# Kernel tuning notes

Measured on AMD Instinct MI355X. Metric: run time of the kernel, lower is better.

The kernel has to match this reference:

```python
import jax, jax.numpy as jnp
import numpy as np

B, D, K, NDIM = 4, 81, 2048, 4  # batch, feature dim, n mixture components, box coord dims


def setup_inputs() -> dict:
    key = jax.random.key(0)
    k1, k2, k3, k4 = jax.random.split(key, 4)
    x = jax.random.normal(k1, (B, D, K), dtype=jnp.float32)
    # mixture weights, positive and normalized over components
    pi = jax.nn.softmax(jax.random.normal(k2, (B, 1, K), dtype=jnp.float32), axis=2)
    # component means in [0,1] (normalized box coords)
    mu = jax.random.uniform(k3, (B, NDIM, K), dtype=jnp.float32)
    # positive scales
    sig = jax.random.uniform(k4, (B, NDIM, K), dtype=jnp.float32) * 0.1 + 0.01
    return {"x": x, "pi": pi, "mu": mu, "sig": sig}


def _cauchy_pdf(mu, sig, points):
    # mu, sig: (B, 1, NDIM, K); points: (B, P, NDIM, 1)
    d = points - mu
    return sig / (jnp.pi * (d * d + sig * sig))


def reference(x, pi, mu, sig):
    # points = mu.transpose(1,2): evaluate the mixture at each component mean
    points = jnp.transpose(mu, (0, 2, 1))            # (B, K, NDIM)
    comp = _cauchy_pdf(mu[:, None, :, :], sig[:, None, :, :],
                       points[:, :, :, None])        # (B, K, NDIM, K)
    comp = jnp.prod(comp, axis=2)                    # independent dims -> (B, K, K)
    lh = pi * comp                                   # pi (B,1,K) broadcasts over points
    coef = lh / jnp.sum(lh, axis=2, keepdims=True)   # normalize over components
    coef = jax.lax.stop_gradient(coef)               # coef_detach=True
    y = jnp.einsum('bdk,bkm->bdm', x, coef)          # torch.bmm(x, coef)
    return y
```

## Files before the change

### kernel.cpp

```cpp
#include <hip/hip_runtime.h>


typedef float v4f __attribute__((ext_vector_type(4)));
typedef float f32x4 __attribute__((ext_vector_type(4)));
typedef short bf16x8 __attribute__((ext_vector_type(8)));

namespace {
constexpr int BB = 4;
constexpr int DD = 81;
constexpr int KK = 2048;
constexpr int MROWS = 96;
constexpr float INV_PI4 = 1.0f / 97.40909103400243f;

constexpr size_t OFF_XBF = 0;
constexpr size_t OFF_RSP = (size_t)BB * MROWS * KK * 2;
}

__device__ __forceinline__ unsigned short f2bf(float f) {
    union { float f; unsigned int u; } v; v.f = f;
    unsigned int u = v.u;
    unsigned int r = (u + 0x7FFFu + ((u >> 16) & 1u)) >> 16;
    return (unsigned short)r;
}

__global__ __launch_bounds__(256, 4) void rowsum_kernel(const float* __restrict__ pi_,
                                                        const float* __restrict__ mu,
                                                        const float* __restrict__ sig,
                                                        float* __restrict__ rowsumPart) {
    __shared__ v4f   mush[256];
    __shared__ v4f   s2sh[256];
    __shared__ float csh[256];
    __shared__ float red[4][64];

    int blk = blockIdx.x;
    int b   = blk >> 8;
    int pc  = (blk & 255) >> 3;
    int ms  = blk & 7;
    int p0  = pc * 64;
    int m0  = ms * 256;
    int t   = threadIdx.x;
    int lane = t & 63, w = t >> 6;

    const float* mub = mu  + (size_t)b * 4 * KK;
    const float* sgb = sig + (size_t)b * 4 * KK;
    const float* pib = pi_ + (size_t)b * KK;

    {
        int m = m0 + t;
        v4f mm = {mub[m], mub[KK + m], mub[2 * KK + m], mub[3 * KK + m]};
        v4f sg = {sgb[m], sgb[KK + m], sgb[2 * KK + m], sgb[3 * KK + m]};
        mush[t] = mm;
        s2sh[t] = sg * sg;
        csh[t]  = pib[m] * ((sg.x * sg.y) * (sg.z * sg.w)) * INV_PI4;
    }
    int p = p0 + lane;
    v4f mp = {mub[p], mub[KK + p], mub[2 * KK + p], mub[3 * KK + p]};
    __syncthreads();

    float sum = 0.f;
#pragma unroll 8
    for (int i = 0; i < 64; ++i) {
        int mi = w * 64 + i;
        v4f d = mp - mush[mi];
        v4f q = d * d + s2sh[mi];
        float den = (q.x * q.y) * (q.z * q.w);
        sum += csh[mi] * __builtin_amdgcn_rcpf(den);
    }

    red[w][lane] = sum;
    __syncthreads();
    if (t < 64)
        rowsumPart[((size_t)(b * 8 + ms)) * KK + p0 + t] =
            red[0][t] + red[1][t] + red[2][t] + red[3][t];
}

__global__ __launch_bounds__(256) void xbf_kernel(const float* __restrict__ x,
                                                  const float* __restrict__ rowsumPart,
                                                  unsigned short* __restrict__ xbf) {
    int d = blockIdx.x;
    int b = blockIdx.y;
    int t = threadIdx.x;
    unsigned short* orow = xbf + ((size_t)(b * MROWS + d)) * KK;
    const float* xrow = x + ((size_t)(b * DD + d)) * KK;
    const float* rsp  = rowsumPart + (size_t)b * 8 * KK;
#pragma unroll
    for (int j = 0; j < 8; ++j) {
        int p = j * 256 + t;
        float rs = 0.f;
#pragma unroll
        for (int s = 0; s < 8; ++s) rs += rsp[(size_t)s * KK + p];
        float v = 0.f;
        if (d < DD) v = xrow[p] * __builtin_amdgcn_rcpf(rs);
        orow[p] = f2bf(v);
    }
}

__global__ __launch_bounds__(512, 2) void gemm_kernel(const float* __restrict__ pi_,
                                                      const float* __restrict__ mu,
                                                      const float* __restrict__ sig,
                                                      const unsigned short* __restrict__ xbf,
                                                      float* __restrict__ out) {
    __shared__ __align__(16) char smem2[49152];
    v4f* mus = (v4f*)smem2;
    f32x4 (*red)[6][64] = (f32x4 (*)[6][64])smem2;

    int t = threadIdx.x;
    int w = t >> 6, lane = t & 63;
    int r = lane & 15, q = lane >> 4;
    int b  = blockIdx.y;
    int m0 = blockIdx.x * 16;

    const float* mub = mu  + (size_t)b * 4 * KK;
    const float* sgb = sig + (size_t)b * 4 * KK;

    for (int i = t; i < KK; i += 512)
        mus[i] = (v4f){mub[i], mub[KK + i], mub[2 * KK + i], mub[3 * KK + i]};

    int m = m0 + r;
    v4f mm = {mub[m], mub[KK + m], mub[2 * KK + m], mub[3 * KK + m]};
    v4f sg = {sgb[m], sgb[KK + m], sgb[2 * KK + m], sgb[3 * KK + m]};
    v4f s2 = sg * sg;
    float cm = pi_[(size_t)b * KK + m] * ((sg.x * sg.y) * (sg.z * sg.w)) * INV_PI4;

    const unsigned short* Abase = xbf + ((size_t)(b * MROWS + r)) * KK;

    f32x4 acc[6];
#pragma unroll
    for (int i = 0; i < 6; ++i) acc[i] = (f32x4)0.f;

    __syncthreads();

    int pw = w * 256;

    bf16x8 Af[6];
#pragma unroll
    for (int Mt = 0; Mt < 6; ++Mt)
        Af[Mt] = *(const bf16x8*)(Abase + (size_t)Mt * 16 * KK + pw + q * 8);

#pragma unroll
    for (int ks = 0; ks < 8; ++ks) {
        int pb = pw + ks * 32 + q * 8;

        bf16x8 Afn[6];
        if (ks < 7) {
            int pbn = pb + 32;
#pragma unroll
            for (int Mt = 0; Mt < 6; ++Mt)
                Afn[Mt] = *(const bf16x8*)(Abase + (size_t)Mt * 16 * KK + pbn);
        }

        bf16x8 Bf;
#pragma unroll
        for (int j = 0; j < 8; ++j) {
            v4f mp = mus[pb + j];
            v4f dd = mp - mm;
            v4f qq = dd * dd + s2;
            float den = (qq.x * qq.y) * (qq.z * qq.w);
            float lh = cm * __builtin_amdgcn_rcpf(den);
            Bf[j] = (short)f2bf(lh);
        }

#pragma unroll
        for (int Mt = 0; Mt < 6; ++Mt)
            acc[Mt] = __builtin_amdgcn_mfma_f32_16x16x32_bf16(Af[Mt], Bf, acc[Mt], 0, 0, 0);

        if (ks < 7) {
#pragma unroll
            for (int Mt = 0; Mt < 6; ++Mt)
                Af[Mt] = Afn[Mt];
        }
    }

    __syncthreads();
#pragma unroll
    for (int Mt = 0; Mt < 6; ++Mt)
        red[w][Mt][lane] = acc[Mt];
    __syncthreads();

    int col = t & 15;
    int dr  = t >> 4;
#pragma unroll
    for (int k = 0; k < 3; ++k) {
        int d = dr + 32 * k;
        if (d < DD) {
            int Mt  = d >> 4;
            int row = d & 15;
            int l   = (row >> 2) * 16 + col;
            int j   = row & 3;
            float s = 0.f;
#pragma unroll
            for (int ww = 0; ww < 8; ++ww) s += red[ww][Mt][l][j];
            out[((size_t)(b * DD + d)) * KK + m0 + col] = s;
        }
    }
}

extern "C" void kernel_launch(void* const* d_in, const int* in_sizes, int n_in,
                              void* d_out, int out_size, void* d_ws, size_t ws_size,
                              hipStream_t stream) {
    const float* x   = (const float*)d_in[0];
    const float* pi_ = (const float*)d_in[1];
    const float* mu  = (const float*)d_in[2];
    const float* sig = (const float*)d_in[3];
    float* out = (float*)d_out;

    unsigned short* xbf = (unsigned short*)((char*)d_ws + OFF_XBF);
    float* rowsumPart   = (float*)((char*)d_ws + OFF_RSP);

    rowsum_kernel<<<1024, 256, 0, stream>>>(pi_, mu, sig, rowsumPart);
    dim3 xg(MROWS, BB);
    xbf_kernel<<<xg, 256, 0, stream>>>(x, rowsumPart, xbf);
    dim3 gg(KK / 16, BB);
    gemm_kernel<<<gg, 512, 0, stream>>>(pi_, mu, sig, xbf, out);
}
```

Baseline: 100.9 us.

## Fuse rowsum and x-normalization into one prep kernel per 16-point tile

Replaces the separate rowsum kernel (partial sums written to workspace) and the xbf scaling kernel with a single prep kernel. Each block owns 16 points, loops over all 2048 components in chunks staged through shared memory, reduces the row sum in shared memory, then scales and converts the matching x columns to bf16. This drops one launch and the partial-sum round trip through global memory. In exchange each block reloads all mu/sig/pi, and the x reads and bf16 writes become strided per 16-column tile, which coalesces less well.

```diff
diff --git a/kernel.cpp b/kernel.cpp
--- a/kernel.cpp
+++ b/kernel.cpp
@@ -13,7 +13,6 @@
 constexpr float INV_PI4 = 1.0f / 97.40909103400243f;
 
 constexpr size_t OFF_XBF = 0;
-constexpr size_t OFF_RSP = (size_t)BB * MROWS * KK * 2;
 }
 
 __device__ __forceinline__ unsigned short f2bf(float f) {
@@ -23,75 +22,72 @@
     return (unsigned short)r;
 }
 
-__global__ __launch_bounds__(256, 4) void rowsum_kernel(const float* __restrict__ pi_,
-                                                        const float* __restrict__ mu,
-                                                        const float* __restrict__ sig,
-                                                        float* __restrict__ rowsumPart) {
+__global__ __launch_bounds__(256) void prep_kernel(const float* __restrict__ x,
+                                                   const float* __restrict__ pi_,
+                                                   const float* __restrict__ mu,
+                                                   const float* __restrict__ sig,
+                                                   unsigned short* __restrict__ xbf) {
     __shared__ v4f   mush[256];
     __shared__ v4f   s2sh[256];
     __shared__ float csh[256];
-    __shared__ float red[4][64];
-
-    int blk = blockIdx.x;
-    int b   = blk >> 8;
-    int pc  = (blk & 255) >> 3;
-    int ms  = blk & 7;
-    int p0  = pc * 64;
-    int m0  = ms * 256;
-    int t   = threadIdx.x;
-    int lane = t & 63, w = t >> 6;
+    __shared__ float sums[16][17];
+    __shared__ float invr[16];
+
+    int b  = blockIdx.y;
+    int p0 = blockIdx.x * 16;
+    int t  = threadIdx.x;
+    int pl = t & 15;
+    int mg = t >> 4;
 
     const float* mub = mu  + (size_t)b * 4 * KK;
     const float* sgb = sig + (size_t)b * 4 * KK;
     const float* pib = pi_ + (size_t)b * KK;
 
-    {
-        int m = m0 + t;
-        v4f mm = {mub[m], mub[KK + m], mub[2 * KK + m], mub[3 * KK + m]};
-        v4f sg = {sgb[m], sgb[KK + m], sgb[2 * KK + m], sgb[3 * KK + m]};
-        mush[t] = mm;
-        s2sh[t] = sg * sg;
-        csh[t]  = pib[m] * ((sg.x * sg.y) * (sg.z * sg.w)) * INV_PI4;
-    }
-    int p = p0 + lane;
+    int p = p0 + pl;
     v4f mp = {mub[p], mub[KK + p], mub[2 * KK + p], mub[3 * KK + p]};
-    __syncthreads();
 
     float sum = 0.f;
-#pragma unroll 8
-    for (int i = 0; i < 64; ++i) {
-        int mi = w * 64 + i;
-        v4f d = mp - mush[mi];
-        v4f q = d * d + s2sh[mi];
-        float den = (q.x * q.y) * (q.z * q.w);
-        sum += csh[mi] * __builtin_amdgcn_rcpf(den);
-    }
-
-    red[w][lane] = sum;
-    __syncthreads();
-    if (t < 64)
-        rowsumPart[((size_t)(b * 8 + ms)) * KK + p0 + t] =
-            red[0][t] + red[1][t] + red[2][t] + red[3][t];
-}
-
-__global__ __launch_bounds__(256) void xbf_kernel(const float* __restrict__ x,
-                                                  const float* __restrict__ rowsumPart,
-                                                  unsigned short* __restrict__ xbf) {
-    int d = blockIdx.x;
-    int b = blockIdx.y;
-    int t = threadIdx.x;
-    unsigned short* orow = xbf + ((size_t)(b * MROWS + d)) * KK;
-    const float* xrow = x + ((size_t)(b * DD + d)) * KK;
-    const float* rsp  = rowsumPart + (size_t)b * 8 * KK;
-#pragma unroll
-    for (int j = 0; j < 8; ++j) {
-        int p = j * 256 + t;
-        float rs = 0.f;
-#pragma unroll
-        for (int s = 0; s < 8; ++s) rs += rsp[(size_t)s * KK + p];
+    for (int c = 0; c < 8; ++c) {
+        int m0 = c * 256;
+        {
+            int m = m0 + t;
+            v4f mm = {mub[m], mub[KK + m], mub[2 * KK + m], mub[3 * KK + m]};
+            v4f sg = {sgb[m], sgb[KK + m], sgb[2 * KK + m], sgb[3 * KK + m]};
+            mush[t] = mm;
+            s2sh[t] = sg * sg;
+            csh[t]  = pib[m] * ((sg.x * sg.y) * (sg.z * sg.w)) * INV_PI4;
+        }
+        __syncthreads();
+#pragma unroll
+        for (int j = 0; j < 16; ++j) {
+            int mi = mg * 16 + j;
+            v4f d = mp - mush[mi];
+            v4f q = d * d + s2sh[mi];
+            float den = (q.x * q.y) * (q.z * q.w);
+            sum += csh[mi] * __builtin_amdgcn_rcpf(den);
+        }
+        __syncthreads();
+    }
+
+    sums[mg][pl] = sum;
+    __syncthreads();
+    if (t < 16) {
+        float s = 0.f;
+#pragma unroll
+        for (int g = 0; g < 16; ++g) s += sums[g][t];
+        invr[t] = __builtin_amdgcn_rcpf(s);
+    }
+    __syncthreads();
+
+    float ir = invr[pl];
+    unsigned short* ob = xbf + ((size_t)b * MROWS) * KK + p0 + pl;
+    const float* xb = x + ((size_t)b * DD) * KK + p0 + pl;
+#pragma unroll
+    for (int k = 0; k < 6; ++k) {
+        int d = mg + 16 * k;
         float v = 0.f;
-        if (d < DD) v = xrow[p] * __builtin_amdgcn_rcpf(rs);
-        orow[p] = f2bf(v);
+        if (d < DD) v = xb[(size_t)d * KK] * ir;
+        ob[(size_t)d * KK] = f2bf(v);
     }
 }
 
@@ -152,8 +148,8 @@
         bf16x8 Bf;
 #pragma unroll
         for (int j = 0; j < 8; ++j) {
-            v4f mp = mus[pb + j];
-            v4f dd = mp - mm;
+            v4f mpv = mus[pb + j];
+            v4f dd = mpv - mm;
             v4f qq = dd * dd + s2;
             float den = (qq.x * qq.y) * (qq.z * qq.w);
             float lh = cm * __builtin_amdgcn_rcpf(den);
@@ -205,11 +201,9 @@
     float* out = (float*)d_out;
 
     unsigned short* xbf = (unsigned short*)((char*)d_ws + OFF_XBF);
-    float* rowsumPart   = (float*)((char*)d_ws + OFF_RSP);
-
-    rowsum_kernel<<<1024, 256, 0, stream>>>(pi_, mu, sig, rowsumPart);
-    dim3 xg(MROWS, BB);
-    xbf_kernel<<<xg, 256, 0, stream>>>(x, rowsumPart, xbf);
+
+    dim3 pg(KK / 16, BB);
+    prep_kernel<<<pg, 256, 0, stream>>>(x, pi_, mu, sig, xbf);
     dim3 gg(KK / 16, BB);
     gemm_kernel<<<gg, 512, 0, stream>>>(pi_, mu, sig, xbf, out);
 }
```

New measurement: 101.9 us. About the same (+1.0%).
